# Optimization experiments

Measured on AMD Instinct MI355X. Metric: run time of the kernel, lower is better.

The kernel has to match this reference:

```python
import jax, jax.numpy as jnp
import numpy as np

N, D, V = 4096, 256, 32000
B, T = 32, 256
U_DECAY, X_DECAY = 0.97, 0.97
EPS = 1e-6


def layernorm_row(z):
    # matches torch: (z - mean) / (std + eps), std with Bessel correction (ddof=1)
    m = jnp.mean(z, axis=-1, keepdims=True)
    s = jnp.std(z, axis=-1, keepdims=True, ddof=1)
    return (z - m) / (s + EPS)


def setup_inputs() -> dict:
    key = jax.random.key(0)
    k1, k2, k3, k4, k5 = jax.random.split(key, 5)
    token_emb = jax.random.normal(k1, (V, D), jnp.float32) / np.float32(np.sqrt(D))
    E = jax.random.normal(k2, (D, N), jnp.float32) / np.float32(np.sqrt(N))
    Dx = jax.random.normal(k3, (N, D), jnp.float32) / np.float32(np.sqrt(D))
    Dy = jax.random.normal(k4, (N, D), jnp.float32) / np.float32(np.sqrt(D))
    idx = jax.random.randint(k5, (B, T), 0, V)
    return {"idx": idx, "token_emb": token_emb, "E": E, "Dx": Dx, "Dy": Dy}


def reference(idx, token_emb, E, Dx, Dy):
    b = idx.shape[0]

    def step(carry, tok):
        x, rho = carry                                   # x: (b,n), rho: (b,d,n)
        v_prev = token_emb[tok]                          # (b,d) embedding gather
        x_t = X_DECAY * x + jax.nn.relu(v_prev @ Dx.T)   # (b,n)
        x_t = x_t / (jnp.sum(jnp.abs(x_t), axis=-1, keepdims=True) + EPS)  # L1 normalize
        a_star = jnp.einsum('bdn,bn->bd', rho, x_t)      # fast-weight readout
        y_t = jax.nn.relu(layernorm_row(a_star) @ Dy.T) * jax.nn.relu(x_t)  # (b,n)
        v_star = layernorm_row(y_t @ E.T)                # (b,d)
        # Hebbian decayed outer-product memory update
        rho = U_DECAY * (rho + jnp.einsum('bd,bn->bdn', layernorm_row(v_prev), x_t))
        return (x_t, rho), v_star

    x0 = jnp.zeros((b, N), jnp.float32)
    rho0 = jnp.zeros((b, D, N), jnp.float32)
    (_, _), vs = jax.lax.scan(step, (x0, rho0), idx.T)   # vs: (T,b,d)
    return jnp.transpose(vs, (1, 0, 2))                  # (b,T,d)
```

## Files before the change

### kernel.cpp

```cpp
#include <hip/hip_runtime.h>
#include <hip/hip_bf16.h>

#define NN 4096
#define DD 256
#define BB 32
#define TT 256
#define EPS 1e-6f
#define DECAY 0.97f
#define LOG2_DECAY -0.043943348f

typedef __hip_bfloat16 bf16;
typedef short short8 __attribute__((ext_vector_type(8)));
typedef float floatx4 __attribute__((ext_vector_type(4)));

__device__ __forceinline__ float bfu2f(short u) {
    return __uint_as_float(((unsigned)(unsigned short)u) << 16);
}

__device__ __forceinline__ float blk_sum_256(float v, volatile float* s4) {
#pragma unroll
    for (int o = 32; o > 0; o >>= 1) v += __shfl_down(v, o, 64);
    int lane = threadIdx.x & 63, w = threadIdx.x >> 6;
    __syncthreads();
    if (lane == 0) s4[w] = v;
    __syncthreads();
    return s4[0] + s4[1] + s4[2] + s4[3];
}

__device__ __forceinline__ void gl16(const bf16* g, bf16* l) {
    __builtin_amdgcn_global_load_lds((const __attribute__((address_space(1))) void*)g,
                                     (__attribute__((address_space(3))) void*)l, 16, 0, 0);
}

__global__ void k_detect(const unsigned short* __restrict__ raw, int* __restrict__ flag) {
    __shared__ int cnt[4];
    int tid = threadIdx.x;
    int bad = 0;
    for (int i = tid; i < 8192; i += 256) {
        unsigned int u = raw[2 * i];
        float v = __uint_as_float(u << 16);
        if (!(fabsf(v) < 1e6f)) bad++;
    }
#pragma unroll
    for (int o = 32; o > 0; o >>= 1) bad += __shfl_down(bad, o, 64);
    int lane = tid & 63, w = tid >> 6;
    if (lane == 0) cnt[w] = bad;
    __syncthreads();
    if (tid == 0) flag[0] = (cnt[0] + cnt[1] + cnt[2] + cnt[3] < 32) ? 1 : 0;
}

__global__ __launch_bounds__(256) void k_convert3(const void* __restrict__ s0,
                                                  const void* __restrict__ s1,
                                                  const void* __restrict__ s2,
                                                  bf16* __restrict__ d0,
                                                  bf16* __restrict__ d1,
                                                  bf16* __restrict__ d2,
                                                  const int* __restrict__ flag) {
    const int per = NN * DD / 8;
    int i = blockIdx.x * 256 + threadIdx.x;
    int m = i / per, j = i % per;
    const void* s = (m == 0) ? s0 : (m == 1) ? s1 : s2;
    bf16* d = (m == 0) ? d0 : (m == 1) ? d1 : d2;
    if (flag[0]) {
        ((uint4*)d)[j] = ((const uint4*)s)[j];
    } else {
        const float4* f = (const float4*)s;
        float4 a = f[2 * j], b = f[2 * j + 1];
        short8 o;
        float va[8] = {a.x, a.y, a.z, a.w, b.x, b.y, b.z, b.w};
#pragma unroll
        for (int k = 0; k < 8; k++) {
            bf16 t = __float2bfloat16(va[k]);
            o[k] = *reinterpret_cast<short*>(&t);
        }
        ((short8*)d)[j] = o;
    }
}

__global__ __launch_bounds__(256) void k_gather_ln(const void* __restrict__ emb,
                                                   const int* __restrict__ idx,
                                                   bf16* __restrict__ Vpb,
                                                   bf16* __restrict__ Ub,
                                                   const int* __restrict__ flag) {
    __shared__ float s4[4];
    int r = blockIdx.x, d = threadIdx.x;
    int tok = idx[r];
    long o = (long)tok * DD + d;
    float e = flag[0] ? __bfloat162float(((const bf16*)emb)[o]) : ((const float*)emb)[o];
    Vpb[(long)r * DD + d] = __float2bfloat16(e);
    float m = blk_sum_256(e, s4) * (1.0f / DD);
    float zc = e - m;
    float var = blk_sum_256(zc * zc, s4) * (1.0f / (DD - 1));
    Ub[(long)r * DD + d] = __float2bfloat16(zc / (sqrtf(fmaxf(var, 0.f)) + EPS));
}

__global__ __launch_bounds__(256) void k_transpose(const bf16* __restrict__ Ub,
                                                   bf16* __restrict__ Ut) {
    __shared__ bf16 tile[32][33];
    int b = blockIdx.z;
    int t0 = blockIdx.x * 32, d0 = blockIdx.y * 32;
    const bf16* src = Ub + (long)b * TT * DD;
    bf16* dst = Ut + (long)b * DD * TT;
    int rr = threadIdx.x >> 3, c4 = (threadIdx.x & 7) * 4;
#pragma unroll
    for (int i = 0; i < 4; i++) tile[rr][c4 + i] = src[(long)(t0 + rr) * DD + d0 + c4 + i];
    __syncthreads();
#pragma unroll
    for (int i = 0; i < 4; i++) dst[(long)(d0 + rr) * TT + t0 + c4 + i] = tile[c4 + i][rr];
}

enum { EPI_RELU_BF16 = 0, EPI_NONE_F32 = 1, EPI_RELU_MULX_BF16 = 2 };

template <int EPI>
__global__ __launch_bounds__(256) void k_fullk(const bf16* __restrict__ A,
                                               const bf16* __restrict__ B,
                                               bf16* __restrict__ C,
                                               const bf16* __restrict__ Xaux,
                                               float* __restrict__ Wsum) {
    __shared__ __align__(16) char smem[65536];
    bf16* As = (bf16*)smem;
    bf16* R = (bf16*)smem;

    int bx = blockIdx.x, by = blockIdx.y;
    {
        int gx = gridDim.x;
        int nwg = gx * gridDim.y;
        int id = by * gx + bx;
        int q = nwg >> 3;
        int nid = (id & 7) * q + (id >> 3);
        bx = nid % gx;
        by = nid / gx;
    }
    int bm = by * 128, bn = bx * 128;
    int tid = threadIdx.x, w = tid >> 6, lane = tid & 63;
    int wm = (w >> 1) * 64, wn = (w & 1) * 64;
    int lm = lane & 15, kh = lane >> 4;

    {
        const bf16* Ab = A + (long)bm * DD;
#pragma unroll
        for (int g = 0; g < 16; g++) {
            int idx = g * 256 + tid;
            int row = idx >> 5, s = idx & 31;
            gl16(Ab + (long)row * DD + ((s ^ (row & 7)) << 3), As + idx * 8);
        }
    }

    const bf16* Bw = B + (long)(bn + wn + lm) * DD + kh * 8;
    short8 b0[4], b1[4];
#pragma unroll
    for (int j = 0; j < 4; j++) b0[j] = *(const short8*)(Bw + (long)j * 16 * DD + 0 * 32);
#pragma unroll
    for (int j = 0; j < 4; j++) b1[j] = *(const short8*)(Bw + (long)j * 16 * DD + 1 * 32);

    floatx4 acc[4][4];
#pragma unroll
    for (int i = 0; i < 4; i++)
#pragma unroll
        for (int j = 0; j < 4; j++) acc[i][j] = (floatx4){0.f, 0.f, 0.f, 0.f};

    __syncthreads();

#pragma unroll
    for (int k = 0; k < 8; k++) {
        short8 af[4];
#pragma unroll
        for (int i = 0; i < 4; i++) {
            int r = wm + i * 16 + lm;
            int slot = (4 * k + kh) ^ (r & 7);
            af[i] = *(const short8*)(As + r * 256 + slot * 8);
        }
        if ((k & 1) == 0) {
#pragma unroll
            for (int i = 0; i < 4; i++)
#pragma unroll
                for (int j = 0; j < 4; j++)
                    acc[i][j] = __builtin_amdgcn_mfma_f32_16x16x32_bf16(af[i], b0[j], acc[i][j], 0, 0, 0);
            if (k < 6) {
#pragma unroll
                for (int j = 0; j < 4; j++)
                    b0[j] = *(const short8*)(Bw + (long)j * 16 * DD + (k + 2) * 32);
            }
        } else {
#pragma unroll
            for (int i = 0; i < 4; i++)
#pragma unroll
                for (int j = 0; j < 4; j++)
                    acc[i][j] = __builtin_amdgcn_mfma_f32_16x16x32_bf16(af[i], b1[j], acc[i][j], 0, 0, 0);
            if (k < 6) {
#pragma unroll
                for (int j = 0; j < 4; j++)
                    b1[j] = *(const short8*)(Bw + (long)j * 16 * DD + (k + 2) * 32);
            }
        }
    }

#pragma unroll
    for (int p = 0; p < 2; p++) {
        __syncthreads();
        if ((w >> 1) == p) {
#pragma unroll
            for (int i = 0; i < 4; i++)
#pragma unroll
                for (int j = 0; j < 4; j++)
#pragma unroll
                    for (int r = 0; r < 4; r++) {
                        int rr = i * 16 + kh * 4 + r;
                        int cc = wn + j * 16 + lm;
                        R[rr * 136 + cc] = __float2bfloat16(fmaxf(acc[i][j][r], 0.f));
                    }
        }
        __syncthreads();
#pragma unroll
        for (int it = 0; it < 4; it++) {
            int row_l = it * 16 + (tid >> 4);
            int c8 = (tid & 15) * 8;
            short8 vv = *(const short8*)(R + row_l * 136 + c8);
            int gm = bm + p * 64 + row_l;
            long off = (long)gm * NN + bn + c8;
            if (EPI == EPI_RELU_BF16) {
                *(short8*)(C + off) = vv;
                float s = 0.f;
#pragma unroll
                for (int k = 0; k < 8; k++) s += bfu2f(vv[k]);
#pragma unroll
                for (int o = 8; o > 0; o >>= 1) s += __shfl_down(s, o, 16);
                if ((tid & 15) == 0) atomicAdd(&Wsum[gm], s);
            } else {
                short8 xx = *(const short8*)(Xaux + off);
                short8 oo;
#pragma unroll
                for (int k = 0; k < 8; k++) {
                    float prod = bfu2f(vv[k]) * fmaxf(bfu2f(xx[k]), 0.f);
                    bf16 t = __float2bfloat16(prod);
                    oo[k] = *reinterpret_cast<short*>(&t);
                }
                *(short8*)(C + off) = oo;
            }
        }
    }
}

template <int EPI, int KSPLIT, int TRI, int SWZ>
__global__ __launch_bounds__(256) void k_mfma_nt(int K,
                                                 const bf16* __restrict__ A, int lda, long sA,
                                                 const bf16* __restrict__ B, int ldb, long sB,
                                                 void* __restrict__ Cv, int ldc, long sC,
                                                 const bf16* __restrict__ Xaux,
                                                 float* __restrict__ Wsum) {
    __shared__ __align__(16) char smem[49152];
    bf16* R = (bf16*)smem;

    int z = blockIdx.z;
    int bz = z / KSPLIT, ks = z % KSPLIT;
    A += (long)bz * sA;
    B += (long)bz * sB;
    int bx = blockIdx.x, by = blockIdx.y;
    if (TRI) {
        by = (blockIdx.x >= 1) ? 1 : 0;
        bx = (blockIdx.x == 2) ? 1 : 0;
    }
    if (SWZ) {
        int gx = gridDim.x;
        int nwg = gx * gridDim.y;
        int id = by * gx + bx;
        int q = nwg >> 3;
        int nid = (id & 7) * q + (id >> 3);
        bx = nid % gx;
        by = nid / gx;
    }
    int bm = by * 128, bn = bx * 128;
    int tid = threadIdx.x;
    int srow = tid >> 2;
    int scol = ((((srow >> 1) & 3) ^ (tid & 3)) << 3);
    int w = tid >> 6, lane = tid & 63;
    int wm = (w >> 1) * 64, wn = (w & 1) * 64;
    int lm = lane & 15, kh = lane >> 4;

    floatx4 acc[4][4];
#pragma unroll
    for (int i = 0; i < 4; i++)
#pragma unroll
        for (int j = 0; j < 4; j++) acc[i][j] = (floatx4){0.f, 0.f, 0.f, 0.f};

    int kchunk = K / KSPLIT;
    int kbeg = ks * kchunk, kend = kbeg + kchunk;
    const bf16* gA0 = A + (long)(bm + srow) * lda + scol;
    const bf16* gA1 = gA0 + (long)64 * lda;
    const bf16* gB0 = B + (long)(bn + srow) * ldb + scol;
    const bf16* gB1 = gB0 + (long)64 * ldb;
    int dslot = tid * 8;

#define STAGE_SLOT(SBASE, KK)                          \
    {                                                  \
        bf16* bufA = (bf16*)(SBASE);                   \
        bf16* bufB = bufA + 4096;                      \
        gl16(gA0 + (KK), bufA + dslot);                \
        gl16(gA1 + (KK), bufA + 2048 + dslot);         \
        gl16(gB0 + (KK), bufB + dslot);                \
        gl16(gB1 + (KK), bufB + 2048 + dslot);         \
    }

    STAGE_SLOT(smem, kbeg);
    if (kbeg + 32 < kend) STAGE_SLOT(smem + 16384, kbeg + 32);

    int cur = 0;
    for (int k0 = kbeg; k0 < kend; k0 += 32) {
        __builtin_amdgcn_s_barrier();
        __builtin_amdgcn_sched_barrier(0);
        if (k0 + 64 < kend) {
            int ps = (cur == 0) ? 2 : cur - 1;
            STAGE_SLOT(smem + ps * 16384, k0 + 64);
        }
        int rem = (kend - k0 - 32) >> 5;
        if (rem >= 2)      asm volatile("s_waitcnt vmcnt(8)" ::: "memory");
        else if (rem == 1) asm volatile("s_waitcnt vmcnt(4)" ::: "memory");
        else               asm volatile("s_waitcnt vmcnt(0)" ::: "memory");
        __builtin_amdgcn_s_barrier();
        __builtin_amdgcn_sched_barrier(0);
        bf16* cbA = (bf16*)(smem + cur * 16384);
        bf16* cbB = cbA + 4096;
        short8 af[4], bfr[4];
#pragma unroll
        for (int i = 0; i < 4; i++) {
            int row = wm + i * 16 + lm;
            af[i] = *(const short8*)(cbA + row * 32 + ((((row >> 1) & 3) ^ kh) << 3));
        }
#pragma unroll
        for (int j = 0; j < 4; j++) {
            int row = wn + j * 16 + lm;
            bfr[j] = *(const short8*)(cbB + row * 32 + ((((row >> 1) & 3) ^ kh) << 3));
        }
#pragma unroll
        for (int i = 0; i < 4; i++)
#pragma unroll
            for (int j = 0; j < 4; j++)
                acc[i][j] = __builtin_amdgcn_mfma_f32_16x16x32_bf16(af[i], bfr[j], acc[i][j], 0, 0, 0);
        cur = (cur == 2) ? 0 : cur + 1;
    }
#undef STAGE_SLOT

    if (EPI == EPI_NONE_F32) {
        long cbase = (long)z * sC;
#pragma unroll
        for (int i = 0; i < 4; i++)
#pragma unroll
            for (int j = 0; j < 4; j++)
#pragma unroll
                for (int r = 0; r < 4; r++) {
                    int gm = bm + wm + i * 16 + kh * 4 + r;
                    int gn = bn + wn + j * 16 + lm;
                    ((float*)Cv)[cbase + (long)gm * ldc + gn] = acc[i][j][r];
                }
        return;
    }

#pragma unroll
    for (int p = 0; p < 2; p++) {
        __syncthreads();
        if ((w >> 1) == p) {
#pragma unroll
            for (int i = 0; i < 4; i++)
#pragma unroll
                for (int j = 0; j < 4; j++)
#pragma unroll
                    for (int r = 0; r < 4; r++) {
                        int rr = i * 16 + kh * 4 + r;
                        int cc = wn + j * 16 + lm;
                        R[rr * 136 + cc] = __float2bfloat16(fmaxf(acc[i][j][r], 0.f));
                    }
        }
        __syncthreads();
#pragma unroll
        for (int it = 0; it < 4; it++) {
            int row_l = it * 16 + (tid >> 4);
            int c8 = (tid & 15) * 8;
            short8 vv = *(const short8*)(R + row_l * 136 + c8);
            int gm = bm + p * 64 + row_l;
            long off = (long)gm * ldc + bn + c8;
            if (EPI == EPI_RELU_BF16) {
                *(short8*)((bf16*)Cv + off) = vv;
                float s = 0.f;
#pragma unroll
                for (int k = 0; k < 8; k++) s += bfu2f(vv[k]);
#pragma unroll
                for (int o = 8; o > 0; o >>= 1) s += __shfl_down(s, o, 16);
                if ((tid & 15) == 0) atomicAdd(&Wsum[gm], s);
            } else {
                short8 xx = *(const short8*)(Xaux + off);
                short8 oo;
#pragma unroll
                for (int k = 0; k < 8; k++) {
                    float prod = bfu2f(vv[k]) * fmaxf(bfu2f(xx[k]), 0.f);
                    bf16 t = __float2bfloat16(prod);
                    oo[k] = *reinterpret_cast<short*>(&t);
                }
                *(short8*)((bf16*)Cv + off) = oo;
            }
        }
    }
}

__global__ __launch_bounds__(256) void k_scalar_scan(const float* __restrict__ Wsum,
                                                     float* __restrict__ invS) {
    __shared__ float sw[BB * TT];
    for (int i = threadIdx.x; i < BB * TT; i += 256) sw[i] = Wsum[i];
    __syncthreads();
    int b = threadIdx.x;
    if (b < BB) {
        float sig = 0.f;
        for (int t = 0; t < TT; t++) {
            float S = DECAY * sig + sw[b * TT + t];
            float inv = 1.f / (S + EPS);
            invS[b * TT + t] = inv;
            sig = S * inv;
        }
    }
}

__global__ __launch_bounds__(256) void k_colscan(bf16* __restrict__ W,
                                                 const float* __restrict__ invS) {
    __shared__ float sv[TT];
    int b = blockIdx.y;
    sv[threadIdx.x] = invS[b * TT + threadIdx.x];
    __syncthreads();
    int n = blockIdx.x * 256 + threadIdx.x;
    bf16* p = W + (long)b * TT * NN + n;
    float x = 0.f;
    for (int t = 0; t < TT; t++) {
        float w = __bfloat162float(p[(long)t * NN]);
        x = (DECAY * x + w) * sv[t];
        p[(long)t * NN] = __float2bfloat16(x);
    }
}

__global__ __launch_bounds__(256) void k_reduce_mask(const float* __restrict__ Gp,
                                                     bf16* __restrict__ G) {
    int r = blockIdx.x;
    int b = r >> 8, t = r & 255;
    int s = threadIdx.x;
    long base = ((long)b * 4) * 65536 + (long)t * 256 + s;
    float v = Gp[base] + Gp[base + 65536] + Gp[base + 2 * 65536] + Gp[base + 3 * 65536];
    float o = (s < t) ? v * exp2f((float)(t - s) * LOG2_DECAY) : 0.f;
    G[(long)r * 256 + s] = __float2bfloat16(o);
}

__global__ __launch_bounds__(256) void k_ln_rows(const float* __restrict__ Zp,
                                                 bf16* __restrict__ O) {
    __shared__ float s4[4];
    long r = blockIdx.x;
    int d = threadIdx.x;
    long b = r >> 8, t = r & 255;
    long base = (b * 2) * 65536 + t * 256 + d;
    float z = Zp[base] + Zp[base + 65536];
    float m = blk_sum_256(z, s4) * (1.0f / DD);
    float zc = z - m;
    float var = blk_sum_256(zc * zc, s4) * (1.0f / (DD - 1));
    O[r * DD + d] = __float2bfloat16(zc / (sqrtf(fmaxf(var, 0.f)) + EPS));
}

__global__ __launch_bounds__(256) void k_final_ln(const float* __restrict__ Zp,
                                                  void* __restrict__ out,
                                                  const int* __restrict__ flag) {
    __shared__ float s4[4];
    long r = blockIdx.x;
    int d = threadIdx.x;
    const long SL = (long)8192 * 256;
    long o = r * DD + d;
    float z = Zp[o] + Zp[o + SL] + Zp[o + 2 * SL] + Zp[o + 3 * SL];
    float m = blk_sum_256(z, s4) * (1.0f / DD);
    float zc = z - m;
    float var = blk_sum_256(zc * zc, s4) * (1.0f / (DD - 1));
    float v = zc / (sqrtf(fmaxf(var, 0.f)) + EPS);
    if (flag[0]) ((bf16*)out)[o] = __float2bfloat16(v);
    else ((float*)out)[o] = v;
}

extern "C" void kernel_launch(void* const* d_in, const int* in_sizes, int n_in,
                              void* d_out, int out_size, void* d_ws, size_t ws_size,
                              hipStream_t stream) {
    const int* idx = (const int*)d_in[0];
    const void* emb = d_in[1];
    const void* E = d_in[2];
    const void* Dx = d_in[3];
    const void* Dy = d_in[4];

    char* base = (char*)d_ws;
    size_t off = 0;
    int* flag = (int*)base; off += 1024;
    bf16* Dxb = (bf16*)(base + off); off += (size_t)NN * DD * 2;
    bf16* Dyb = (bf16*)(base + off); off += (size_t)NN * DD * 2;
    bf16* Eb  = (bf16*)(base + off); off += (size_t)DD * NN * 2;
    bf16* Vpb = (bf16*)(base + off); off += (size_t)BB * TT * DD * 2;
    bf16* Ub  = (bf16*)(base + off); off += (size_t)BB * TT * DD * 2;
    bf16* Ut  = (bf16*)(base + off); off += (size_t)BB * TT * DD * 2;
    float* Wsum = (float*)(base + off); off += (size_t)BB * TT * 4;
    float* invS = (float*)(base + off); off += (size_t)BB * TT * 4;
    bf16* ALNb = (bf16*)(base + off); off += (size_t)BB * TT * DD * 2;
    bf16* G = (bf16*)(base + off); off += (size_t)BB * TT * TT * 2;
    float* Gp = (float*)(base + off); off += (size_t)4 * BB * TT * TT * 4;
    float* Astar = Gp;
    float* Zp = Gp;
    bf16* Xb = (bf16*)(base + off); off += (size_t)BB * TT * NN * 2;

    const int M = BB * TT;

    k_detect<<<1, 256, 0, stream>>>((const unsigned short*)emb, flag);
    k_convert3<<<3 * NN * DD / 8 / 256, 256, 0, stream>>>(Dx, Dy, E, Dxb, Dyb, Eb, flag);
    k_gather_ln<<<M, 256, 0, stream>>>(emb, idx, Vpb, Ub, flag);
    k_transpose<<<dim3(8, 8, BB), 256, 0, stream>>>(Ub, Ut);

    hipMemsetAsync(Wsum, 0, (size_t)M * 4, stream);

    k_fullk<EPI_RELU_BF16><<<dim3(32, 64), 256, 0, stream>>>(Vpb, Dxb, Xb, nullptr, Wsum);

    k_scalar_scan<<<1, 256, 0, stream>>>(Wsum, invS);
    k_colscan<<<dim3(16, BB, 1), 256, 0, stream>>>(Xb, invS);

    k_mfma_nt<EPI_NONE_F32, 4, 1, 0><<<dim3(3, 1, BB * 4), 256, 0, stream>>>(
        NN, Xb, NN, (long)TT * NN, Xb, NN, (long)TT * NN, Gp, TT, (long)TT * TT, nullptr, nullptr);
    k_reduce_mask<<<M, 256, 0, stream>>>(Gp, G);

    k_mfma_nt<EPI_NONE_F32, 2, 0, 0><<<dim3(2, 2, BB * 2), 256, 0, stream>>>(
        TT, G, TT, (long)TT * TT, Ut, TT, (long)DD * TT, Astar, DD, (long)TT * DD, nullptr, nullptr);
    k_ln_rows<<<M, 256, 0, stream>>>(Astar, ALNb);

    k_fullk<EPI_RELU_MULX_BF16><<<dim3(32, 64), 256, 0, stream>>>(ALNb, Dyb, Xb, Xb, nullptr);

    k_mfma_nt<EPI_NONE_F32, 4, 0, 1><<<dim3(2, 64, 4), 256, 0, stream>>>(
        NN, Xb, NN, 0, Eb, NN, 0, Zp, DD, (long)M * DD, nullptr, nullptr);

    k_final_ln<<<M, 256, 0, stream>>>(Zp, d_out, flag);
}
```

Measured before the change: 336.4 us.

## Enlarge full-K GEMM tiles to 256x256 with double-buffered LDS staging

Replaces the 128x128 full-K GEMM, which held the whole A tile in LDS and read B straight from global memory, with a 256x256 tile per 512-thread block. A and B are staged in 32-wide K slices through a swizzled, double-buffered LDS pipeline driven by explicit vmcnt waits and barriers. The aim is more operand reuse per block and less global traffic for B. In exchange each thread holds twice as many accumulators, which raises register pressure, and the grid has a quarter as many blocks, which can reduce occupancy and wave balance.

```diff
diff --git a/kernel.cpp b/kernel.cpp
--- a/kernel.cpp
+++ b/kernel.cpp
@@ -112,13 +112,12 @@
 enum { EPI_RELU_BF16 = 0, EPI_NONE_F32 = 1, EPI_RELU_MULX_BF16 = 2 };
 
 template <int EPI>
-__global__ __launch_bounds__(256) void k_fullk(const bf16* __restrict__ A,
-                                               const bf16* __restrict__ B,
-                                               bf16* __restrict__ C,
-                                               const bf16* __restrict__ Xaux,
-                                               float* __restrict__ Wsum) {
+__global__ __launch_bounds__(512, 2) void k_fused256(const bf16* __restrict__ A,
+                                                     const bf16* __restrict__ B,
+                                                     bf16* __restrict__ C,
+                                                     const bf16* __restrict__ Xaux,
+                                                     float* __restrict__ Wsum) {
     __shared__ __align__(16) char smem[65536];
-    bf16* As = (bf16*)smem;
     bf16* R = (bf16*)smem;
 
     int bx = blockIdx.x, by = blockIdx.y;
@@ -131,91 +130,87 @@
         bx = nid % gx;
         by = nid / gx;
     }
-    int bm = by * 128, bn = bx * 128;
-    int tid = threadIdx.x, w = tid >> 6, lane = tid & 63;
-    int wm = (w >> 1) * 64, wn = (w & 1) * 64;
+    int bm = by * 256, bn = bx * 256;
+    int tid = threadIdx.x, wid = tid >> 6, lane = tid & 63;
+    int wr = wid >> 2, wc = wid & 3;
     int lm = lane & 15, kh = lane >> 4;
 
-    {
-        const bf16* Ab = A + (long)bm * DD;
-#pragma unroll
-        for (int g = 0; g < 16; g++) {
-            int idx = g * 256 + tid;
-            int row = idx >> 5, s = idx & 31;
-            gl16(Ab + (long)row * DD + ((s ^ (row & 7)) << 3), As + idx * 8);
-        }
-    }
-
-    const bf16* Bw = B + (long)(bn + wn + lm) * DD + kh * 8;
-    short8 b0[4], b1[4];
-#pragma unroll
-    for (int j = 0; j < 4; j++) b0[j] = *(const short8*)(Bw + (long)j * 16 * DD + 0 * 32);
-#pragma unroll
-    for (int j = 0; j < 4; j++) b1[j] = *(const short8*)(Bw + (long)j * 16 * DD + 1 * 32);
-
-    floatx4 acc[4][4];
-#pragma unroll
-    for (int i = 0; i < 4; i++)
+    int srow2 = tid >> 2;
+    int swzcol = (((tid & 3) ^ ((srow2 >> 1) & 3)) << 3);
+    const bf16* gA0 = A + (long)(bm + srow2) * DD + swzcol;
+    const bf16* gA1 = gA0 + (long)128 * DD;
+    const bf16* gB0 = B + (long)(bn + srow2) * DD + swzcol;
+    const bf16* gB1 = gB0 + (long)128 * DD;
+    int chunk = ((kh ^ ((lm >> 1) & 3)) << 3);
+
+    floatx4 acc[8][4];
+#pragma unroll
+    for (int i = 0; i < 8; i++)
 #pragma unroll
         for (int j = 0; j < 4; j++) acc[i][j] = (floatx4){0.f, 0.f, 0.f, 0.f};
 
-    __syncthreads();
-
-#pragma unroll
-    for (int k = 0; k < 8; k++) {
-        short8 af[4];
-#pragma unroll
-        for (int i = 0; i < 4; i++) {
-            int r = wm + i * 16 + lm;
-            int slot = (4 * k + kh) ^ (r & 7);
-            af[i] = *(const short8*)(As + r * 256 + slot * 8);
-        }
-        if ((k & 1) == 0) {
-#pragma unroll
-            for (int i = 0; i < 4; i++)
+#define STAGE256(SBASE, KK)                             \
+    {                                                   \
+        bf16* As_ = (bf16*)(SBASE);                     \
+        bf16* Bs_ = As_ + 8192;                         \
+        gl16(gA0 + (KK), As_ + tid * 8);                \
+        gl16(gA1 + (KK), As_ + 4096 + tid * 8);         \
+        gl16(gB0 + (KK), Bs_ + tid * 8);                \
+        gl16(gB1 + (KK), Bs_ + 4096 + tid * 8);         \
+    }
+
+    STAGE256(smem, 0);
+
+    int cur = 0;
+#pragma unroll
+    for (int k0 = 0; k0 < 256; k0 += 32) {
+        __builtin_amdgcn_s_barrier();
+        __builtin_amdgcn_sched_barrier(0);
+        if (k0 + 32 < 256) STAGE256(smem + ((cur ^ 1) * 32768), k0 + 32);
+        if (k0 + 32 < 256) asm volatile("s_waitcnt vmcnt(4)" ::: "memory");
+        else               asm volatile("s_waitcnt vmcnt(0)" ::: "memory");
+        __builtin_amdgcn_s_barrier();
+        __builtin_amdgcn_sched_barrier(0);
+        bf16* cbA = (bf16*)(smem + cur * 32768);
+        bf16* cbB = cbA + 8192;
+        short8 af[8], bfr[4];
+#pragma unroll
+        for (int i = 0; i < 8; i++)
+            af[i] = *(const short8*)(cbA + (wr * 128 + i * 16 + lm) * 32 + chunk);
+#pragma unroll
+        for (int j = 0; j < 4; j++)
+            bfr[j] = *(const short8*)(cbB + (wc * 64 + j * 16 + lm) * 32 + chunk);
+#pragma unroll
+        for (int i = 0; i < 8; i++)
+#pragma unroll
+            for (int j = 0; j < 4; j++)
+                acc[i][j] = __builtin_amdgcn_mfma_f32_16x16x32_bf16(af[i], bfr[j], acc[i][j], 0, 0, 0);
+        cur ^= 1;
+    }
+#undef STAGE256
+
+#pragma unroll
+    for (int p = 0; p < 4; p++) {
+        __syncthreads();
+        if (wr == (p >> 1)) {
+            int ibase = (p & 1) * 4;
+#pragma unroll
+            for (int ii = 0; ii < 4; ii++)
 #pragma unroll
                 for (int j = 0; j < 4; j++)
-                    acc[i][j] = __builtin_amdgcn_mfma_f32_16x16x32_bf16(af[i], b0[j], acc[i][j], 0, 0, 0);
-            if (k < 6) {
-#pragma unroll
-                for (int j = 0; j < 4; j++)
-                    b0[j] = *(const short8*)(Bw + (long)j * 16 * DD + (k + 2) * 32);
-            }
-        } else {
-#pragma unroll
-            for (int i = 0; i < 4; i++)
-#pragma unroll
-                for (int j = 0; j < 4; j++)
-                    acc[i][j] = __builtin_amdgcn_mfma_f32_16x16x32_bf16(af[i], b1[j], acc[i][j], 0, 0, 0);
-            if (k < 6) {
-#pragma unroll
-                for (int j = 0; j < 4; j++)
-                    b1[j] = *(const short8*)(Bw + (long)j * 16 * DD + (k + 2) * 32);
-            }
-        }
-    }
-
-#pragma unroll
-    for (int p = 0; p < 2; p++) {
+#pragma unroll
+                    for (int r = 0; r < 4; r++) {
+                        int rr = ii * 16 + kh * 4 + r;
+                        int cc = wc * 64 + j * 16 + lm;
+                        R[rr * 264 + cc] = __float2bfloat16(fmaxf(acc[ibase + ii][j][r], 0.f));
+                    }
+        }
         __syncthreads();
-        if ((w >> 1) == p) {
-#pragma unroll
-            for (int i = 0; i < 4; i++)
-#pragma unroll
-                for (int j = 0; j < 4; j++)
-#pragma unroll
-                    for (int r = 0; r < 4; r++) {
-                        int rr = i * 16 + kh * 4 + r;
-                        int cc = wn + j * 16 + lm;
-                        R[rr * 136 + cc] = __float2bfloat16(fmaxf(acc[i][j][r], 0.f));
-                    }
-        }
-        __syncthreads();
 #pragma unroll
         for (int it = 0; it < 4; it++) {
-            int row_l = it * 16 + (tid >> 4);
-            int c8 = (tid & 15) * 8;
-            short8 vv = *(const short8*)(R + row_l * 136 + c8);
+            int row_l = it * 16 + (tid >> 5);
+            int c8 = (tid & 31) * 8;
+            short8 vv = *(const short8*)(R + row_l * 264 + c8);
             int gm = bm + p * 64 + row_l;
             long off = (long)gm * NN + bn + c8;
             if (EPI == EPI_RELU_BF16) {
@@ -224,8 +219,8 @@
 #pragma unroll
                 for (int k = 0; k < 8; k++) s += bfu2f(vv[k]);
 #pragma unroll
-                for (int o = 8; o > 0; o >>= 1) s += __shfl_down(s, o, 16);
-                if ((tid & 15) == 0) atomicAdd(&Wsum[gm], s);
+                for (int o = 16; o > 0; o >>= 1) s += __shfl_down(s, o, 32);
+                if ((tid & 31) == 0) atomicAdd(&Wsum[gm], s);
             } else {
                 short8 xx = *(const short8*)(Xaux + off);
                 short8 oo;
@@ -512,7 +507,7 @@
 
     hipMemsetAsync(Wsum, 0, (size_t)M * 4, stream);
 
-    k_fullk<EPI_RELU_BF16><<<dim3(32, 64), 256, 0, stream>>>(Vpb, Dxb, Xb, nullptr, Wsum);
+    k_fused256<EPI_RELU_BF16><<<dim3(16, 32), 512, 0, stream>>>(Vpb, Dxb, Xb, nullptr, Wsum);
 
     k_scalar_scan<<<1, 256, 0, stream>>>(Wsum, invS);
     k_colscan<<<dim3(16, BB, 1), 256, 0, stream>>>(Xb, invS);
@@ -525,7 +520,7 @@
         TT, G, TT, (long)TT * TT, Ut, TT, (long)DD * TT, Astar, DD, (long)TT * DD, nullptr, nullptr);
     k_ln_rows<<<M, 256, 0, stream>>>(Astar, ALNb);
 
-    k_fullk<EPI_RELU_MULX_BF16><<<dim3(32, 64), 256, 0, stream>>>(ALNb, Dyb, Xb, Xb, nullptr);
+    k_fused256<EPI_RELU_MULX_BF16><<<dim3(16, 32), 512, 0, stream>>>(ALNb, Dyb, Xb, Xb, nullptr);
 
     k_mfma_nt<EPI_NONE_F32, 4, 0, 1><<<dim3(2, 64, 4), 256, 0, stream>>>(
         NN, Xb, NN, 0, Eb, NN, 0, Zp, DD, (long)M * DD, nullptr, nullptr);
```

After: 312.0 us. 7.2% less time.
